# Kernel tuning notes

Measured on AMD Instinct MI355X. Metric: run time of the kernel, lower is better.

Reference implementation:

```python
import jax, jax.numpy as jnp
import numpy as np

N = 50000      # nodes
E = 800000     # unique directed edges (avg degree 16)
F = 64         # input_dim
D = 64         # output_dim (== F -> residual is identity)
ALPHA = 0.5
LCS_THR = 0.5  # enable_lcs_masking=True, lcs_threshold=0.5


def setup_inputs() -> dict:
    key = jax.random.key(0)
    ks = jax.random.split(key, 16)
    x = jax.random.normal(ks[0], (N, F), jnp.float32)
    src = jax.random.randint(ks[1], (E,), 0, N, jnp.int32)
    dst = jax.random.randint(ks[2], (E,), 0, N, jnp.int32)
    # integer-valued multiplicities in {1,2,3,4} (recurring-transaction counts)
    counts = jnp.floor(jax.random.uniform(ks[3], (E,), jnp.float32) * 4.0) + 1.0
    def lin(k, fan_in, shape):
        return jax.random.normal(k, shape, jnp.float32) / np.float32(np.sqrt(fan_in))
    return dict(
        x=x, counts=counts,
        W_s2d=lin(ks[4], F, (F, D)), b_s2d=jnp.zeros((D,), jnp.float32),
        W_d2s=lin(ks[5], F, (F, D)), b_d2s=jnp.zeros((D,), jnp.float32),
        W_l1=lin(ks[6], 2 * F, (2 * F, F)), b_l1=jnp.zeros((F,), jnp.float32),
        W_l2=lin(ks[7], F, (F, 1)), b_l2=jnp.zeros((1,), jnp.float32),
        W_g1=lin(ks[8], 2 * D, (2 * D, D)), b_g1=jnp.zeros((D,), jnp.float32),
        W_g2=lin(ks[9], D, (D, 1)), b_g2=jnp.zeros((1,), jnp.float32),
        src=src, dst=dst,
    )


def reference(x, counts, W_s2d, b_s2d, W_d2s, b_d2s,
              W_l1, b_l1, W_l2, b_l2, W_g1, b_g1, W_g2, b_g2,
              src, dst):
    # in/out degrees from full (unmasked) multiplicities, clamped at 1
    in_deg = jnp.maximum(jax.ops.segment_sum(counts, dst, num_segments=N), 1.0)
    out_deg = jnp.maximum(jax.ops.segment_sum(counts, src, num_segments=N), 1.0)

    # LCS per unique edge: sigmoid(MLP([x_src, x_dst])), detached in torch
    lcs_in = jnp.concatenate([x[src], x[dst]], axis=-1)          # [E, 2F]
    lcs = jax.nn.sigmoid(
        jax.nn.relu(lcs_in @ W_l1 + b_l1) @ W_l2 + b_l2)[:, 0]   # [E]
    lcs = jax.lax.stop_gradient(lcs)
    keep = (lcs >= LCS_THR).astype(x.dtype)                      # LCS masking

    # symmetric-normalized edge weights with multiplicity counts
    w = counts * keep * jax.lax.rsqrt(out_deg[src] * in_deg[dst])  # [E]

    # direction-aware message passing (redundancy-eliminated, per unique edge)
    h_s2d = x @ W_s2d + b_s2d                                    # [N, D]
    h_d2s = x @ W_d2s + b_d2s                                    # [N, D]
    m_in = jax.ops.segment_sum(w[:, None] * h_s2d[src], dst, num_segments=N)
    m_out = jax.ops.segment_sum(w[:, None] * h_d2s[dst], src, num_segments=N)

    # node-wise gating over inbound vs outbound flows
    gate = jax.nn.sigmoid(
        jax.nn.relu(jnp.concatenate([m_in, m_out], axis=-1) @ W_g1 + b_g1)
        @ W_g2 + b_g2)                                           # [N, 1]

    # gated alpha-blend + identity residual (input_dim == output_dim)
    out = ALPHA * gate * m_in + (1.0 - ALPHA) * (1.0 - gate) * m_out + x
    return out
```

## Files before the change

### kernel.cpp

```cpp
#include <hip/hip_runtime.h>
#include <math.h>


typedef unsigned long long u64;

#define SLOTS 56

__device__ __forceinline__ float bflo(unsigned u) { return __uint_as_float(u << 16); }
__device__ __forceinline__ float bfhi(unsigned u) { return __uint_as_float(u & 0xffff0000u); }
__device__ __forceinline__ unsigned rne16(float f) {
    unsigned u = __float_as_uint(f);
    return (u + 0x7fffu + ((u >> 16) & 1u)) >> 16;
}

__global__ __launch_bounds__(256) void proj_zero_kernel(
    const float* __restrict__ x,
    const float* __restrict__ Wl1,  const float* __restrict__ bl1,
    const float* __restrict__ Ws2d, const float* __restrict__ bs2d,
    const float* __restrict__ Wd2s, const float* __restrict__ bd2s,
    const float* __restrict__ Wg1,  float* __restrict__ Wg1q,
    float* __restrict__ A, float* __restrict__ B,
    unsigned* __restrict__ Ah, unsigned* __restrict__ Bh,
    unsigned* __restrict__ HSh, unsigned* __restrict__ HDh,
    int4* __restrict__ zp4, int nz4, int PB, int N)
{
    if (blockIdx.x >= PB) {
        if (blockIdx.x == PB + 64) {
            for (int i = threadIdx.x; i < 8192; i += 256) {
                const int k = i >> 6, c = i & 63;
                Wg1q[((k >> 2) * 64 + c) * 4 + (k & 3)] = Wg1[i];
            }
            return;
        }
        const int t0 = (blockIdx.x - PB) * 256 + threadIdx.x;
        const int stride = 64 * 256;
        const int4 z = make_int4(0, 0, 0, 0);
        for (int i = t0; i < nz4; i += stride) zp4[i] = z;
        return;
    }
    __shared__ float xs[64][64];
    const int tid  = threadIdx.x;
    const int n0   = blockIdx.x * 64;
    const int wv   = tid >> 6;
    const int cc   = tid & 63;
    const int side = wv & 1;
    const int par  = wv >> 1;

    const float* W0 = side ? (Wl1 + 64 * 64) : Wl1;
    const float* W1 = side ? Wd2s : Ws2d;
    const float  b0 = side ? 0.f : bl1[cc];
    const float  b1 = side ? bd2s[cc] : bs2d[cc];
    float*    oA  = side ? B  : A;
    unsigned* oAh = side ? Bh : Ah;
    unsigned* oH  = side ? HDh : HSh;

    float w0[64], w1[64];
#pragma unroll
    for (int k = 0; k < 64; ++k) {
        w0[k] = W0[k * 64 + cc];
        w1[k] = W1[k * 64 + cc];
    }

#pragma unroll
    for (int j = 0; j < 4; ++j) {
        int f4  = tid + j * 256;
        int row = f4 >> 4;
        int c4  = f4 & 15;
        int gn  = n0 + row;
        float4 v = (gn < N) ? ((const float4*)x)[(long)gn * 16 + c4]
                            : make_float4(0.f, 0.f, 0.f, 0.f);
        ((float4*)&xs[row][0])[c4] = v;
    }
    __syncthreads();

    const int nmax = (N - n0 < 64) ? (N - n0) : 64;
    for (int n = par; n < nmax; n += 2) {
        float a0 = b0, a1 = b1;
#pragma unroll
        for (int k = 0; k < 64; k += 4) {
            float4 xv = *((const float4*)&xs[n][k]);
            a0 += xv.x * w0[k] + xv.y * w0[k + 1] + xv.z * w0[k + 2] + xv.w * w0[k + 3];
            a1 += xv.x * w1[k] + xv.y * w1[k + 1] + xv.z * w1[k + 2] + xv.w * w1[k + 3];
        }
        const long gn = n0 + n;
        oA[gn * 64 + cc] = a0;
        const float p0 = __shfl_xor(a0, 1);
        const float p1 = __shfl_xor(a1, 1);
        if ((cc & 1) == 0) {
            oAh[gn * 32 + (cc >> 1)] = (rne16(p0) << 16) | rne16(a0);
            oH [gn * 32 + (cc >> 1)] = (rne16(p1) << 16) | rne16(a1);
        }
    }
}

#define LCS_MARGIN 0.04f
__global__ __launch_bounds__(256) void edge_w_kernel(
    const int* __restrict__ src, const int* __restrict__ dst,
    const float* __restrict__ counts,
    const float* __restrict__ A, const float* __restrict__ B,
    const unsigned* __restrict__ Ah, const unsigned* __restrict__ Bh,
    const float* __restrict__ Wl2, const float* __restrict__ bl2,
    u64* __restrict__ pk, unsigned* __restrict__ rec, int N, int E)
{
    const int tid = threadIdx.x;
    const int e   = blockIdx.x * 32 + (tid >> 3);
    const int c   = tid & 7;
    if (e >= E) return;

    const int s = src[e];
    const int d = dst[e];
    const uint4  ua  = *((const uint4*)(Ah + (long)s * 32 + c * 4));
    const uint4  ub  = *((const uint4*)(Bh + (long)d * 32 + c * 4));
    const float4 wl0 = *((const float4*)(Wl2 + c * 8));
    const float4 wl1 = *((const float4*)(Wl2 + c * 8 + 4));

    float p = fmaxf(bflo(ua.x) + bflo(ub.x), 0.f) * wl0.x
            + fmaxf(bfhi(ua.x) + bfhi(ub.x), 0.f) * wl0.y
            + fmaxf(bflo(ua.y) + bflo(ub.y), 0.f) * wl0.z
            + fmaxf(bfhi(ua.y) + bfhi(ub.y), 0.f) * wl0.w
            + fmaxf(bflo(ua.z) + bflo(ub.z), 0.f) * wl1.x
            + fmaxf(bfhi(ua.z) + bfhi(ub.z), 0.f) * wl1.y
            + fmaxf(bflo(ua.w) + bflo(ub.w), 0.f) * wl1.z
            + fmaxf(bfhi(ua.w) + bfhi(ub.w), 0.f) * wl1.w;
    p += __shfl_xor(p, 1); p += __shfl_xor(p, 2); p += __shfl_xor(p, 4);

    float z = p + bl2[0];
    if (fabsf(z) < LCS_MARGIN) {
        const float4 a0 = *((const float4*)(A + (long)s * 64 + c * 8));
        const float4 a1 = *((const float4*)(A + (long)s * 64 + c * 8 + 4));
        const float4 b0 = *((const float4*)(B + (long)d * 64 + c * 8));
        const float4 b1 = *((const float4*)(B + (long)d * 64 + c * 8 + 4));
        float q = fmaxf(a0.x + b0.x, 0.f) * wl0.x + fmaxf(a0.y + b0.y, 0.f) * wl0.y
                + fmaxf(a0.z + b0.z, 0.f) * wl0.z + fmaxf(a0.w + b0.w, 0.f) * wl0.w
                + fmaxf(a1.x + b1.x, 0.f) * wl1.x + fmaxf(a1.y + b1.y, 0.f) * wl1.y
                + fmaxf(a1.z + b1.z, 0.f) * wl1.z + fmaxf(a1.w + b1.w, 0.f) * wl1.w;
        q += __shfl_xor(q, 1); q += __shfl_xor(q, 2); q += __shfl_xor(q, 4);
        z = q + bl2[0];
    }

    if (c == 0) {
        const u64 keep = (z >= 0.f) ? 1ull : 0ull;
        const unsigned ic = (unsigned)__float2int_rn(counts[e]);
        const u64 od = atomicAdd(pk + d,     (keep << 32) | (u64)ic);
        const u64 os = atomicAdd(pk + N + s, (keep << 32) | (u64)ic);
        if (keep) {
            rec[(long)d * SLOTS + (int)(od >> 32)]       = ((unsigned)s << 16) | ic;
            rec[(long)(N + s) * SLOTS + (int)(os >> 32)] = ((unsigned)d << 16) | ic;
        }
    }
}

__global__ __launch_bounds__(256) void gather_gate_kernel(
    const u64* __restrict__ pk, const unsigned* __restrict__ rec,
    const unsigned* __restrict__ HSh, const unsigned* __restrict__ HDh,
    const float* __restrict__ x,
    const float* __restrict__ Wg1q, const float* __restrict__ bg1,
    const float* __restrict__ Wg2, const float* __restrict__ bg2,
    float* __restrict__ out, int N)
{
    __shared__ float mbuf[16][128];
    const int tid  = threadIdx.x;
    const int wv   = tid >> 6;
    const int lane = tid & 63;
    const int g    = lane >> 3;
    const int c    = lane & 7;
    const int nb   = blockIdx.x * 16 + wv * 4;

    const unsigned* pklo = (const unsigned*)pk;

    for (int j = 0; j < 4; ++j) {
        const int n   = nb + j;
        const int row = wv * 4 + j;
        if (n >= N) {
            if (g == 0) {
#pragma unroll
                for (int q = 0; q < 8; ++q) {
                    mbuf[row][c * 8 + q]      = 0.f;
                    mbuf[row][64 + c * 8 + q] = 0.f;
                }
            }
            continue;
        }

        const u64 pin  = pk[n];
        const u64 pout = pk[N + n];
        const int ei = (int)(pin >> 32);
        const int eo = (int)(pout >> 32);
        const float qin  = rsqrtf(fmaxf((float)(unsigned)pin,  1.f));
        const float qout = rsqrtf(fmaxf((float)(unsigned)pout, 1.f));
        const unsigned* rin  = rec + (long)n * SLOTS;
        const unsigned* rout = rec + (long)(N + n) * SLOTS;

        float mi[8], mo[8];
#pragma unroll
        for (int q = 0; q < 8; ++q) { mi[q] = 0.f; mo[q] = 0.f; }

        for (int ii = g; ii < ei; ii += 8) {
            const unsigned ra = rin[ii];
            const unsigned sa = ra >> 16;
            const float dga = (float)pklo[2 * (N + (int)sa)];
            const float wa  = (float)(ra & 0xFFu) * rsqrtf(fmaxf(dga, 1.f));
            const uint4 ua = *((const uint4*)(HSh + (long)sa * 32 + c * 4));
            mi[0] += wa * bflo(ua.x);  mi[1] += wa * bfhi(ua.x);
            mi[2] += wa * bflo(ua.y);  mi[3] += wa * bfhi(ua.y);
            mi[4] += wa * bflo(ua.z);  mi[5] += wa * bfhi(ua.z);
            mi[6] += wa * bflo(ua.w);  mi[7] += wa * bfhi(ua.w);
        }
        for (int jo = g; jo < eo; jo += 8) {
            const unsigned rb = rout[jo];
            const unsigned sb = rb >> 16;
            const float dgb = (float)pklo[2 * (int)sb];
            const float wb  = (float)(rb & 0xFFu) * rsqrtf(fmaxf(dgb, 1.f));
            const uint4 ub = *((const uint4*)(HDh + (long)sb * 32 + c * 4));
            mo[0] += wb * bflo(ub.x);  mo[1] += wb * bfhi(ub.x);
            mo[2] += wb * bflo(ub.y);  mo[3] += wb * bfhi(ub.y);
            mo[4] += wb * bflo(ub.z);  mo[5] += wb * bfhi(ub.z);
            mo[6] += wb * bflo(ub.w);  mo[7] += wb * bfhi(ub.w);
        }

#pragma unroll
        for (int q = 0; q < 8; ++q) {
            mi[q] += __shfl_xor(mi[q], 8);
            mi[q] += __shfl_xor(mi[q], 16);
            mi[q] += __shfl_xor(mi[q], 32);
            mo[q] += __shfl_xor(mo[q], 8);
            mo[q] += __shfl_xor(mo[q], 16);
            mo[q] += __shfl_xor(mo[q], 32);
        }
        if (g == 0) {
#pragma unroll
            for (int q = 0; q < 8; ++q) {
                mbuf[row][c * 8 + q]      = mi[q] * qin;
                mbuf[row][64 + c * 8 + q] = mo[q] * qout;
            }
        }
    }

    const float bgv = bg1[lane];
    float ac0 = bgv, ac1 = bgv, ac2 = bgv, ac3 = bgv;
    const float* m0 = &mbuf[wv * 4 + 0][0];
    const float* m1 = &mbuf[wv * 4 + 1][0];
    const float* m2 = &mbuf[wv * 4 + 2][0];
    const float* m3 = &mbuf[wv * 4 + 3][0];
#pragma unroll 4
    for (int k4 = 0; k4 < 32; ++k4) {
        const float4 w4 = ((const float4*)Wg1q)[k4 * 64 + lane];
        const float4 q0 = ((const float4*)m0)[k4];
        const float4 q1 = ((const float4*)m1)[k4];
        const float4 q2 = ((const float4*)m2)[k4];
        const float4 q3 = ((const float4*)m3)[k4];
        ac0 += q0.x * w4.x + q0.y * w4.y + q0.z * w4.z + q0.w * w4.w;
        ac1 += q1.x * w4.x + q1.y * w4.y + q1.z * w4.z + q1.w * w4.w;
        ac2 += q2.x * w4.x + q2.y * w4.y + q2.z * w4.z + q2.w * w4.w;
        ac3 += q3.x * w4.x + q3.y * w4.y + q3.z * w4.z + q3.w * w4.w;
    }
    const float wg2 = Wg2[lane];
    float v0 = fmaxf(ac0, 0.f) * wg2;
    float v1 = fmaxf(ac1, 0.f) * wg2;
    float v2 = fmaxf(ac2, 0.f) * wg2;
    float v3 = fmaxf(ac3, 0.f) * wg2;
#pragma unroll
    for (int m = 1; m <= 32; m <<= 1) {
        v0 += __shfl_xor(v0, m);
        v1 += __shfl_xor(v1, m);
        v2 += __shfl_xor(v2, m);
        v3 += __shfl_xor(v3, m);
    }
    const float bb = bg2[0];
    float gt[4];
    gt[0] = 1.f / (1.f + expf(-(v0 + bb)));
    gt[1] = 1.f / (1.f + expf(-(v1 + bb)));
    gt[2] = 1.f / (1.f + expf(-(v2 + bb)));
    gt[3] = 1.f / (1.f + expf(-(v3 + bb)));

#pragma unroll
    for (int j = 0; j < 4; ++j) {
        const int n = nb + j;
        if (n >= N) continue;
        const float miv = mbuf[wv * 4 + j][lane];
        const float mov = mbuf[wv * 4 + j][64 + lane];
        out[(long)n * 64 + lane] = 0.5f * gt[j] * miv + 0.5f * (1.f - gt[j]) * mov
                                 + x[(long)n * 64 + lane];
    }
}

extern "C" void kernel_launch(void* const* d_in, const int* in_sizes, int n_in,
                              void* d_out, int out_size, void* d_ws, size_t ws_size,
                              hipStream_t stream) {
    const float* x      = (const float*)d_in[0];
    const float* counts = (const float*)d_in[1];
    const float* Ws2d   = (const float*)d_in[2];
    const float* bs2d   = (const float*)d_in[3];
    const float* Wd2s   = (const float*)d_in[4];
    const float* bd2s   = (const float*)d_in[5];
    const float* Wl1    = (const float*)d_in[6];
    const float* bl1    = (const float*)d_in[7];
    const float* Wl2    = (const float*)d_in[8];
    const float* bl2    = (const float*)d_in[9];
    const float* Wg1    = (const float*)d_in[10];
    const float* bg1    = (const float*)d_in[11];
    const float* Wg2    = (const float*)d_in[12];
    const float* bg2    = (const float*)d_in[13];
    const int*   src    = (const int*)d_in[14];
    const int*   dst    = (const int*)d_in[15];

    const int N  = in_sizes[0] / 64;
    const int E  = in_sizes[14];
    const int PB = (N + 63) / 64;

    float* ws      = (float*)d_ws;
    float* Wg1q    = ws;
    float* A       = ws + 8192;
    float* B       = A + 64L * N;
    unsigned* Ah   = (unsigned*)(B + 64L * N);
    unsigned* Bh   = Ah + 32L * N;
    unsigned* HSh  = Bh + 32L * N;
    unsigned* HDh  = HSh + 32L * N;
    u64* pk        = (u64*)(HDh + 32L * N);
    unsigned* rec  = (unsigned*)(pk + 2L * N);

    proj_zero_kernel<<<PB + 65, 256, 0, stream>>>(
        x, Wl1, bl1, Ws2d, bs2d, Wd2s, bd2s, Wg1, Wg1q,
        A, B, Ah, Bh, HSh, HDh, (int4*)pk, N, PB, N);

    edge_w_kernel<<<(E + 31) / 32, 256, 0, stream>>>(
        src, dst, counts, A, B, Ah, Bh, Wl2, bl2, pk, rec, N, E);

    gather_gate_kernel<<<(N + 15) / 16, 256, 0, stream>>>(
        pk, rec, HSh, HDh, x, Wg1q, bg1, Wg2, bg2, (float*)d_out, N);
}
```

Measured before the change: 275.3 us.

## Move s2d/d2s projections into edge kernel blocks to overlap with edge scoring

The first kernel now computes only the LCS-layer projections (A/B and their bf16 copies). The message projections HSh/HDh are computed by extra blocks appended to the edge-weight kernel's grid. Those projection blocks can run alongside the memory-bound edge gather work instead of serializing before it. This halves the register weight arrays in the first kernel. The cost is that the edge kernel now declares 16KB of static shared memory, which edge blocks do not use but which may limit their occupancy.

```diff
diff --git a/kernel.cpp b/kernel.cpp
--- a/kernel.cpp
+++ b/kernel.cpp
@@ -5,6 +5,7 @@
 typedef unsigned long long u64;
 
 #define SLOTS 56
+#define LCS_MARGIN 0.04f
 
 __device__ __forceinline__ float bflo(unsigned u) { return __uint_as_float(u << 16); }
 __device__ __forceinline__ float bfhi(unsigned u) { return __uint_as_float(u & 0xffff0000u); }
@@ -13,15 +14,12 @@
     return (u + 0x7fffu + ((u >> 16) & 1u)) >> 16;
 }
 
-__global__ __launch_bounds__(256) void proj_zero_kernel(
+__global__ __launch_bounds__(256) void projAB_zero_kernel(
     const float* __restrict__ x,
-    const float* __restrict__ Wl1,  const float* __restrict__ bl1,
-    const float* __restrict__ Ws2d, const float* __restrict__ bs2d,
-    const float* __restrict__ Wd2s, const float* __restrict__ bd2s,
-    const float* __restrict__ Wg1,  float* __restrict__ Wg1q,
+    const float* __restrict__ Wl1, const float* __restrict__ bl1,
+    const float* __restrict__ Wg1, float* __restrict__ Wg1q,
     float* __restrict__ A, float* __restrict__ B,
     unsigned* __restrict__ Ah, unsigned* __restrict__ Bh,
-    unsigned* __restrict__ HSh, unsigned* __restrict__ HDh,
     int4* __restrict__ zp4, int nz4, int PB, int N)
 {
     if (blockIdx.x >= PB) {
@@ -46,20 +44,14 @@
     const int side = wv & 1;
     const int par  = wv >> 1;
 
-    const float* W0 = side ? (Wl1 + 64 * 64) : Wl1;
-    const float* W1 = side ? Wd2s : Ws2d;
-    const float  b0 = side ? 0.f : bl1[cc];
-    const float  b1 = side ? bd2s[cc] : bs2d[cc];
+    const float* W  = side ? (Wl1 + 64 * 64) : Wl1;
+    const float  bv = side ? 0.f : bl1[cc];
     float*    oA  = side ? B  : A;
     unsigned* oAh = side ? Bh : Ah;
-    unsigned* oH  = side ? HDh : HSh;
-
-    float w0[64], w1[64];
-#pragma unroll
-    for (int k = 0; k < 64; ++k) {
-        w0[k] = W0[k * 64 + cc];
-        w1[k] = W1[k * 64 + cc];
-    }
+
+    float w[64];
+#pragma unroll
+    for (int k = 0; k < 64; ++k) w[k] = W[k * 64 + cc];
 
 #pragma unroll
     for (int j = 0; j < 4; ++j) {
@@ -75,36 +67,80 @@
 
     const int nmax = (N - n0 < 64) ? (N - n0) : 64;
     for (int n = par; n < nmax; n += 2) {
-        float a0 = b0, a1 = b1;
+        float a0 = bv;
 #pragma unroll
         for (int k = 0; k < 64; k += 4) {
             float4 xv = *((const float4*)&xs[n][k]);
-            a0 += xv.x * w0[k] + xv.y * w0[k + 1] + xv.z * w0[k + 2] + xv.w * w0[k + 3];
-            a1 += xv.x * w1[k] + xv.y * w1[k + 1] + xv.z * w1[k + 2] + xv.w * w1[k + 3];
+            a0 += xv.x * w[k] + xv.y * w[k + 1] + xv.z * w[k + 2] + xv.w * w[k + 3];
         }
         const long gn = n0 + n;
         oA[gn * 64 + cc] = a0;
         const float p0 = __shfl_xor(a0, 1);
-        const float p1 = __shfl_xor(a1, 1);
-        if ((cc & 1) == 0) {
+        if ((cc & 1) == 0)
             oAh[gn * 32 + (cc >> 1)] = (rne16(p0) << 16) | rne16(a0);
-            oH [gn * 32 + (cc >> 1)] = (rne16(p1) << 16) | rne16(a1);
-        }
-    }
-}
-
-#define LCS_MARGIN 0.04f
-__global__ __launch_bounds__(256) void edge_w_kernel(
+    }
+}
+
+__global__ __launch_bounds__(256) void edge_proj_kernel(
     const int* __restrict__ src, const int* __restrict__ dst,
     const float* __restrict__ counts,
     const float* __restrict__ A, const float* __restrict__ B,
     const unsigned* __restrict__ Ah, const unsigned* __restrict__ Bh,
     const float* __restrict__ Wl2, const float* __restrict__ bl2,
-    u64* __restrict__ pk, unsigned* __restrict__ rec, int N, int E)
+    u64* __restrict__ pk, unsigned* __restrict__ rec,
+    const float* __restrict__ x,
+    const float* __restrict__ Ws2d, const float* __restrict__ bs2d,
+    const float* __restrict__ Wd2s, const float* __restrict__ bd2s,
+    unsigned* __restrict__ HSh, unsigned* __restrict__ HDh,
+    int EB, int N, int E)
 {
+    __shared__ float xs[64][64];
     const int tid = threadIdx.x;
-    const int e   = blockIdx.x * 32 + (tid >> 3);
-    const int c   = tid & 7;
+
+    if (blockIdx.x >= EB) {
+        const int n0   = (blockIdx.x - EB) * 64;
+        const int wv   = tid >> 6;
+        const int cc   = tid & 63;
+        const int side = wv & 1;
+        const int par  = wv >> 1;
+
+        const float* W  = side ? Wd2s : Ws2d;
+        const float  bv = side ? bd2s[cc] : bs2d[cc];
+        unsigned* oH = side ? HDh : HSh;
+
+        float w[64];
+#pragma unroll
+        for (int k = 0; k < 64; ++k) w[k] = W[k * 64 + cc];
+
+#pragma unroll
+        for (int j = 0; j < 4; ++j) {
+            int f4  = tid + j * 256;
+            int row = f4 >> 4;
+            int c4  = f4 & 15;
+            int gn  = n0 + row;
+            float4 v = (gn < N) ? ((const float4*)x)[(long)gn * 16 + c4]
+                                : make_float4(0.f, 0.f, 0.f, 0.f);
+            ((float4*)&xs[row][0])[c4] = v;
+        }
+        __syncthreads();
+
+        const int nmax = (N - n0 < 64) ? (N - n0) : 64;
+        for (int n = par; n < nmax; n += 2) {
+            float a0 = bv;
+#pragma unroll
+            for (int k = 0; k < 64; k += 4) {
+                float4 xv = *((const float4*)&xs[n][k]);
+                a0 += xv.x * w[k] + xv.y * w[k + 1] + xv.z * w[k + 2] + xv.w * w[k + 3];
+            }
+            const float p0 = __shfl_xor(a0, 1);
+            if ((cc & 1) == 0)
+                oH[((long)(n0 + n)) * 32 + (cc >> 1)] = (rne16(p0) << 16) | rne16(a0);
+        }
+        return;
+    }
+
+    const int e = blockIdx.x * 32 + (tid >> 3);
+    const int c = tid & 7;
     if (e >= E) return;
 
     const int s = src[e];
@@ -307,6 +343,7 @@
     const int N  = in_sizes[0] / 64;
     const int E  = in_sizes[14];
     const int PB = (N + 63) / 64;
+    const int EB = (E + 31) / 32;
 
     float* ws      = (float*)d_ws;
     float* Wg1q    = ws;
@@ -319,12 +356,12 @@
     u64* pk        = (u64*)(HDh + 32L * N);
     unsigned* rec  = (unsigned*)(pk + 2L * N);
 
-    proj_zero_kernel<<<PB + 65, 256, 0, stream>>>(
-        x, Wl1, bl1, Ws2d, bs2d, Wd2s, bd2s, Wg1, Wg1q,
-        A, B, Ah, Bh, HSh, HDh, (int4*)pk, N, PB, N);
-
-    edge_w_kernel<<<(E + 31) / 32, 256, 0, stream>>>(
-        src, dst, counts, A, B, Ah, Bh, Wl2, bl2, pk, rec, N, E);
+    projAB_zero_kernel<<<PB + 65, 256, 0, stream>>>(
+        x, Wl1, bl1, Wg1, Wg1q, A, B, Ah, Bh, (int4*)pk, N, PB, N);
+
+    edge_proj_kernel<<<EB + PB, 256, 0, stream>>>(
+        src, dst, counts, A, B, Ah, Bh, Wl2, bl2, pk, rec,
+        x, Ws2d, bs2d, Wd2s, bd2s, HSh, HDh, EB, N, E);
 
     gather_gate_kernel<<<(N + 15) / 16, 256, 0, stream>>>(
         pk, rec, HSh, HDh, x, Wg1q, bg1, Wg2, bg2, (float*)d_out, N);
```

Measured after the change: 280.8 us. No clear change (+2.0%).
